# Kernel tuning notes

Measured on AMD Instinct MI355X. Metric: run time of the kernel, lower is better.

The kernel has to match this reference:

```python
import jax, jax.numpy as jnp
import numpy as np

B, L, D_MODEL, EXPAND, HEADDIM, QK_DIM = 2, 512, 512, 2, 128, 16
D_INNER = EXPAND * D_MODEL            # 1024
NHEADS = D_INNER // HEADDIM           # 8
EPS = 1e-3
STD_DEV = 1.0 / np.sqrt(2 * L * QK_DIM)
TWO_PI = 2.0 * np.pi


def setup_inputs() -> dict:
    key = jax.random.key(0)
    kv, kq, kk = jax.random.split(key, 3)
    v = jax.random.normal(kv, (B, L, D_INNER), dtype=jnp.float32)
    q = jax.random.normal(kq, (B, L, NHEADS * QK_DIM), dtype=jnp.float32)
    k = jax.random.normal(kk, (B, L, NHEADS * QK_DIM), dtype=jnp.float32)
    return {"v": v, "q": q, "k": k}


def reference(v, q, k):
    b, l, dim = v.shape
    residual = v
    # b l (n h) -> b l n h
    vh = v.reshape(b, l, NHEADS, HEADDIM)
    # b l (n d) -> b n d l
    qh = q.reshape(b, l, NHEADS, QK_DIM).transpose(0, 2, 3, 1)
    kh = k.reshape(b, l, NHEADS, QK_DIM).transpose(0, 2, 3, 1)
    pos = jnp.arange(l, dtype=v.dtype)  # position indices
    c = jnp.asarray(TWO_PI * EPS, dtype=v.dtype)
    # q_matrix[b,n,d,t,l] = cos(c * q[b,n,d,t] * pos[l])
    q_mat = jnp.cos(c * qh[:, :, :, :, None] * pos)
    # k_matrix[b,n,d,l,t] = cos(c * k[b,n,d,t] * pos[l])
    k_mat = jnp.cos(c * kh[:, :, :, None, :] * pos[:, None])
    sym = (q_mat - k_mat).sum(axis=2)  # (b, n, t, l)
    out = jnp.einsum('bntl,blnh->btnh', sym, vh)
    out = jnp.asarray(STD_DEV, v.dtype) * out
    return out.reshape(b, l, dim) + residual
```

## Files before the change

kernel.cpp:

```cpp
#include <hip/hip_runtime.h>

#define L_SEQ   512
#define NHEADS_ 8
#define HEADDIM_ 128
#define QKD     16
#define DINNER  1024
#define EPS_F   1e-3f
#define STD_F   0.0078125f

typedef __attribute__((ext_vector_type(8))) short  short8;
typedef __attribute__((ext_vector_type(4))) float  floatx4;

__device__ __forceinline__ float cosrev(float rev) {
    float r = rev - floorf(rev);
    return __builtin_amdgcn_cosf(r);
}

__device__ __forceinline__ unsigned short f2bf_rne(float x) {
    union { float f; unsigned int u; } v;
    v.f = x;
    unsigned int r = v.u + 0x7fffu + ((v.u >> 16) & 1u);
    return (unsigned short)(r >> 16);
}
__device__ __forceinline__ unsigned short f2bf_fast(float x) {
    union { float f; unsigned int u; } v;
    v.f = x;
    return (unsigned short)((v.u + 0x8000u) >> 16);
}

__global__ __launch_bounds__(256) void prep_kernel(const float* __restrict__ v,
                                                   const float* __restrict__ k,
                                                   unsigned short* __restrict__ vt,
                                                   float* __restrict__ ks) {
    const int bid = blockIdx.x;
    const int tid = threadIdx.x;
    if (bid < 512) {
        const int bn = bid & 15, tc = (bid >> 4) & 15, lh = bid >> 8;
        const int b = bn >> 3, n = bn & 7;
        const int l = lh * 256 + tid;
        const float t0f = (float)(tc * 32);
        const float* krow = k + ((size_t)(b * L_SEQ + l)) * (NHEADS_ * QKD) + n * QKD;
        float M[16], C1[16], C0[16];
#pragma unroll
        for (int d4 = 0; d4 < 4; ++d4) {
            float4 kk = *(const float4*)(krow + 4 * d4);
            float dl[4] = {EPS_F * kk.x, EPS_F * kk.y, EPS_F * kk.z, EPS_F * kk.w};
#pragma unroll
            for (int e = 0; e < 4; ++e) {
                int d = d4 * 4 + e;
                M[d]  = 2.f * cosrev(dl[e]);
                C1[d] = cosrev(dl[e] * t0f);
                C0[d] = cosrev(dl[e] * (t0f - 1.f));
            }
        }
        float* kout = ks + ((size_t)bn * L_SEQ) * L_SEQ + (size_t)(tc * 32) * L_SEQ + l;
#pragma unroll
        for (int m = 0; m < 32; ++m) {
            float s0 = (C1[0] + C1[1]) + (C1[2] + C1[3]);
            float s1 = (C1[4] + C1[5]) + (C1[6] + C1[7]);
            float s2 = (C1[8] + C1[9]) + (C1[10] + C1[11]);
            float s3 = (C1[12] + C1[13]) + (C1[14] + C1[15]);
            kout[(size_t)m * L_SEQ] = (s0 + s1) + (s2 + s3);
#pragma unroll
            for (int d = 0; d < 16; ++d) {
                float nx = fmaf(M[d], C1[d], -C0[d]);
                C0[d] = C1[d];
                C1[d] = nx;
            }
        }
    } else {
        const int bid2 = bid - 512;
        const int l0 = (bid2 & 7) * 64;
        const int h0 = ((bid2 >> 3) & 1) * 64;
        const int bn = bid2 >> 4;
        const int b = bn >> 3, n = bn & 7;
        __shared__ float tile[64][65];
        const float* vb = v + ((size_t)b * L_SEQ) * DINNER + n * HEADDIM_;
#pragma unroll
        for (int i = 0; i < 16; ++i) {
            int f = i * 256 + tid;
            int hh = f & 63, ll = f >> 6;
            tile[hh][ll] = vb[(size_t)(l0 + ll) * DINNER + (h0 + hh)];
        }
        __syncthreads();
        unsigned short* vrow = vt + ((size_t)bn * HEADDIM_) * L_SEQ;
#pragma unroll
        for (int i = 0; i < 16; ++i) {
            int f = i * 256 + tid;
            int ll = f & 63, hh = f >> 6;
            vrow[(size_t)(h0 + hh) * L_SEQ + (l0 + ll)] = f2bf_rne(tile[hh][ll]);
        }
    }
}

__global__ __launch_bounds__(256, 2) void vand_main(const float* __restrict__ v,
                                                    const float* __restrict__ q,
                                                    const unsigned short* __restrict__ vt,
                                                    const float* __restrict__ ks,
                                                    float* __restrict__ out) {
    const int tid  = threadIdx.x;
    const int w    = tid >> 6;
    const int lane = tid & 63;
    const int tl   = lane & 15;
    const int quad = lane >> 4;
    const int ttile = blockIdx.x;
    const int bn    = blockIdx.y;
    const int b = bn >> 3, n = bn & 7;

    const int   t   = ttile * 16 + tl;
    const int   l0  = w * 128 + quad * 32;
    const float l0f = (float)l0;

    const float* qrow = q + ((size_t)(b * L_SEQ + t)) * (NHEADS_ * QKD) + n * QKD;
    float M[16], C1[16], C0[16];
#pragma unroll
    for (int d4 = 0; d4 < 4; ++d4) {
        float4 qq = *(const float4*)(qrow + 4 * d4);
        float dl[4] = {EPS_F * qq.x, EPS_F * qq.y, EPS_F * qq.z, EPS_F * qq.w};
#pragma unroll
        for (int e = 0; e < 4; ++e) {
            int d = d4 * 4 + e;
            M[d]  = 2.f * cosrev(dl[e]);
            C1[d] = cosrev(dl[e] * l0f);
            C0[d] = cosrev(dl[e] * (l0f - 1.f));
        }
    }

    const unsigned short* vrow  = vt + ((size_t)bn * HEADDIM_) * L_SEQ;
    const float*          ksrow = ks + ((size_t)(bn * L_SEQ + t)) * L_SEQ + l0;

    floatx4 acc[8] = {};

#pragma unroll
    for (int c = 0; c < 4; ++c) {
        float4 kv0 = *(const float4*)(ksrow + c * 8);
        float4 kv1 = *(const float4*)(ksrow + c * 8 + 4);
        const float kvv[8] = {kv0.x, kv0.y, kv0.z, kv0.w, kv1.x, kv1.y, kv1.z, kv1.w};
        short8 af;
#pragma unroll
        for (int jj = 0; jj < 8; ++jj) {
            float s0 = (C1[0] + C1[1]) + (C1[2] + C1[3]);
            float s1 = (C1[4] + C1[5]) + (C1[6] + C1[7]);
            float s2 = (C1[8] + C1[9]) + (C1[10] + C1[11]);
            float s3 = (C1[12] + C1[13]) + (C1[14] + C1[15]);
            float s  = ((s0 + s1) + (s2 + s3)) - kvv[jj];
            af[jj] = (short)f2bf_fast(s);
#pragma unroll
            for (int d = 0; d < 16; ++d) {
                float nx = fmaf(M[d], C1[d], -C0[d]);
                C0[d] = C1[d];
                C1[d] = nx;
            }
        }
#pragma unroll
        for (int ht = 0; ht < 8; ++ht) {
            const short8 bfr = *(const short8*)((const short*)vrow +
                                  (size_t)(ht * 16 + tl) * L_SEQ + l0 + c * 8);
            acc[ht] = __builtin_amdgcn_mfma_f32_16x16x32_bf16(af, bfr, acc[ht], 0, 0, 0);
        }
    }

    __shared__ float red[4][64][33];
#pragma unroll
    for (int ht = 0; ht < 8; ++ht)
#pragma unroll
        for (int r = 0; r < 4; ++r)
            red[w][lane][ht * 4 + r] = acc[ht][r];
    __syncthreads();

    const float* vbase = v   + ((size_t)b * L_SEQ) * DINNER + n * HEADDIM_;
    float*       obase = out + ((size_t)b * L_SEQ) * DINNER + n * HEADDIM_;
#pragma unroll
    for (int i = 0; i < 8; ++i) {
        int e    = i * 256 + tid;
        int h    = e & 127;
        int tloc = e >> 7;
        int lidx = ((tloc >> 2) << 4) + (h & 15);
        int aidx = ((h >> 4) << 2) + (tloc & 3);
        float sum = red[0][lidx][aidx] + red[1][lidx][aidx]
                  + red[2][lidx][aidx] + red[3][lidx][aidx];
        size_t gi = (size_t)(ttile * 16 + tloc) * DINNER + h;
        obase[gi] = vbase[gi] + STD_F * sum;
    }
}

extern "C" void kernel_launch(void* const* d_in, const int* in_sizes, int n_in,
                              void* d_out, int out_size, void* d_ws, size_t ws_size,
                              hipStream_t stream) {
    const float* v = (const float*)d_in[0];
    const float* q = (const float*)d_in[1];
    const float* k = (const float*)d_in[2];
    float* out = (float*)d_out;
    unsigned short* vt = (unsigned short*)d_ws;
    float* ks = (float*)((char*)d_ws + (2u << 20));

    prep_kernel<<<dim3(768), 256, 0, stream>>>(v, k, vt, ks);
    vand_main<<<dim3(L_SEQ / 16, 16), 256, 0, stream>>>(v, q, vt, ks, out);
}
```

Before: 84.79 us.

## Fuse k-cosine sum into main kernel via LDS and use packed float2 recurrences

Removes the global ks intermediate, about 16 MB of fp32 written and then read back. Each main block now computes its own 16 rows of the k-side cosine sums into padded shared memory. The Chebyshev recurrences are rewritten on float2 vectors so the compiler can emit packed FMA instructions. In exchange, k-side work is recomputed per block tile and LDS use grows by about 34 KB, which may reduce occupancy.

Result: faster. 77.31 us (-8.8%).

```diff
diff --git a/kernel.cpp b/kernel.cpp
--- a/kernel.cpp
+++ b/kernel.cpp
@@ -8,8 +8,11 @@
 #define EPS_F   1e-3f
 #define STD_F   0.0078125f
 
+#define KS_ROW  529
+
 typedef __attribute__((ext_vector_type(8))) short  short8;
 typedef __attribute__((ext_vector_type(4))) float  floatx4;
+typedef __attribute__((ext_vector_type(2))) float  float2v;
 
 __device__ __forceinline__ float cosrev(float rev) {
     float r = rev - floorf(rev);
@@ -28,76 +31,37 @@
     return (unsigned short)((v.u + 0x8000u) >> 16);
 }
 
-__global__ __launch_bounds__(256) void prep_kernel(const float* __restrict__ v,
-                                                   const float* __restrict__ k,
-                                                   unsigned short* __restrict__ vt,
-                                                   float* __restrict__ ks) {
+__global__ __launch_bounds__(256) void vtrans_kernel(const float* __restrict__ v,
+                                                     unsigned short* __restrict__ vt) {
     const int bid = blockIdx.x;
     const int tid = threadIdx.x;
-    if (bid < 512) {
-        const int bn = bid & 15, tc = (bid >> 4) & 15, lh = bid >> 8;
-        const int b = bn >> 3, n = bn & 7;
-        const int l = lh * 256 + tid;
-        const float t0f = (float)(tc * 32);
-        const float* krow = k + ((size_t)(b * L_SEQ + l)) * (NHEADS_ * QKD) + n * QKD;
-        float M[16], C1[16], C0[16];
+    const int l0 = (bid & 7) * 64;
+    const int h0 = ((bid >> 3) & 1) * 64;
+    const int bn = bid >> 4;
+    const int b = bn >> 3, n = bn & 7;
+    __shared__ float tile[64][65];
+    const float* vb = v + ((size_t)b * L_SEQ) * DINNER + n * HEADDIM_;
 #pragma unroll
-        for (int d4 = 0; d4 < 4; ++d4) {
-            float4 kk = *(const float4*)(krow + 4 * d4);
-            float dl[4] = {EPS_F * kk.x, EPS_F * kk.y, EPS_F * kk.z, EPS_F * kk.w};
+    for (int i = 0; i < 16; ++i) {
+        int f = i * 256 + tid;
+        int hh = f & 63, ll = f >> 6;
+        tile[hh][ll] = vb[(size_t)(l0 + ll) * DINNER + (h0 + hh)];
+    }
+    __syncthreads();
+    unsigned short* vrow = vt + ((size_t)bn * HEADDIM_) * L_SEQ;
 #pragma unroll
-            for (int e = 0; e < 4; ++e) {
-                int d = d4 * 4 + e;
-                M[d]  = 2.f * cosrev(dl[e]);
-                C1[d] = cosrev(dl[e] * t0f);
-                C0[d] = cosrev(dl[e] * (t0f - 1.f));
-            }
-        }
-        float* kout = ks + ((size_t)bn * L_SEQ) * L_SEQ + (size_t)(tc * 32) * L_SEQ + l;
-#pragma unroll
-        for (int m = 0; m < 32; ++m) {
-            float s0 = (C1[0] + C1[1]) + (C1[2] + C1[3]);
-            float s1 = (C1[4] + C1[5]) + (C1[6] + C1[7]);
-            float s2 = (C1[8] + C1[9]) + (C1[10] + C1[11]);
-            float s3 = (C1[12] + C1[13]) + (C1[14] + C1[15]);
-            kout[(size_t)m * L_SEQ] = (s0 + s1) + (s2 + s3);
-#pragma unroll
-            for (int d = 0; d < 16; ++d) {
-                float nx = fmaf(M[d], C1[d], -C0[d]);
-                C0[d] = C1[d];
-                C1[d] = nx;
-            }
-        }
-    } else {
-        const int bid2 = bid - 512;
-        const int l0 = (bid2 & 7) * 64;
-        const int h0 = ((bid2 >> 3) & 1) * 64;
-        const int bn = bid2 >> 4;
-        const int b = bn >> 3, n = bn & 7;
-        __shared__ float tile[64][65];
-        const float* vb = v + ((size_t)b * L_SEQ) * DINNER + n * HEADDIM_;
-#pragma unroll
-        for (int i = 0; i < 16; ++i) {
-            int f = i * 256 + tid;
-            int hh = f & 63, ll = f >> 6;
-            tile[hh][ll] = vb[(size_t)(l0 + ll) * DINNER + (h0 + hh)];
-        }
-        __syncthreads();
-        unsigned short* vrow = vt + ((size_t)bn * HEADDIM_) * L_SEQ;
-#pragma unroll
-        for (int i = 0; i < 16; ++i) {
-            int f = i * 256 + tid;
-            int ll = f & 63, hh = f >> 6;
-            vrow[(size_t)(h0 + hh) * L_SEQ + (l0 + ll)] = f2bf_rne(tile[hh][ll]);
-        }
+    for (int i = 0; i < 16; ++i) {
+        int f = i * 256 + tid;
+        int ll = f & 63, hh = f >> 6;
+        vrow[(size_t)(h0 + hh) * L_SEQ + (l0 + ll)] = f2bf_rne(tile[hh][ll]);
     }
 }
 
-__global__ __launch_bounds__(256, 2) void vand_main(const float* __restrict__ v,
-                                                    const float* __restrict__ q,
-                                                    const unsigned short* __restrict__ vt,
-                                                    const float* __restrict__ ks,
-                                                    float* __restrict__ out) {
+__global__ __launch_bounds__(256, 2) void vand_fused(const float* __restrict__ v,
+                                                     const float* __restrict__ q,
+                                                     const float* __restrict__ k,
+                                                     const unsigned short* __restrict__ vt,
+                                                     float* __restrict__ out) {
     const int tid  = threadIdx.x;
     const int w    = tid >> 6;
     const int lane = tid & 63;
@@ -106,50 +70,88 @@
     const int ttile = blockIdx.x;
     const int bn    = blockIdx.y;
     const int b = bn >> 3, n = bn & 7;
+    const float t0f = (float)(ttile * 16);
+
+    __shared__ float ksl[16 * KS_ROW];
+    __shared__ float red[4][64][33];
+
+#pragma unroll
+    for (int rep = 0; rep < 2; ++rep) {
+        const int l = tid + rep * 256;
+        const float* krow = k + ((size_t)(b * L_SEQ + l)) * (NHEADS_ * QKD) + n * QKD;
+        float kk[16];
+#pragma unroll
+        for (int d4 = 0; d4 < 4; ++d4) {
+            float4 t4 = *(const float4*)(krow + 4 * d4);
+            kk[d4 * 4 + 0] = t4.x; kk[d4 * 4 + 1] = t4.y;
+            kk[d4 * 4 + 2] = t4.z; kk[d4 * 4 + 3] = t4.w;
+        }
+        float2v M2[8], C1[8], C0[8];
+#pragma unroll
+        for (int i = 0; i < 8; ++i) {
+            float a0 = EPS_F * kk[2 * i], a1 = EPS_F * kk[2 * i + 1];
+            M2[i].x = 2.f * cosrev(a0);          M2[i].y = 2.f * cosrev(a1);
+            C1[i].x = cosrev(a0 * t0f);          C1[i].y = cosrev(a1 * t0f);
+            C0[i].x = cosrev(a0 * (t0f - 1.f));  C0[i].y = cosrev(a1 * (t0f - 1.f));
+        }
+        const int base = (l >> 5) * 33 + (l & 31);
+#pragma unroll
+        for (int m = 0; m < 16; ++m) {
+            float2v s = ((C1[0] + C1[1]) + (C1[2] + C1[3]))
+                      + ((C1[4] + C1[5]) + (C1[6] + C1[7]));
+            ksl[m * KS_ROW + base] = s.x + s.y;
+#pragma unroll
+            for (int i = 0; i < 8; ++i) {
+                float2v nx = M2[i] * C1[i] - C0[i];
+                C0[i] = C1[i];
+                C1[i] = nx;
+            }
+        }
+    }
+    __syncthreads();
 
     const int   t   = ttile * 16 + tl;
     const int   l0  = w * 128 + quad * 32;
     const float l0f = (float)l0;
 
     const float* qrow = q + ((size_t)(b * L_SEQ + t)) * (NHEADS_ * QKD) + n * QKD;
-    float M[16], C1[16], C0[16];
+    float2v M2[8], C1[8], C0[8];
 #pragma unroll
     for (int d4 = 0; d4 < 4; ++d4) {
         float4 qq = *(const float4*)(qrow + 4 * d4);
-        float dl[4] = {EPS_F * qq.x, EPS_F * qq.y, EPS_F * qq.z, EPS_F * qq.w};
+        float aa[4] = {EPS_F * qq.x, EPS_F * qq.y, EPS_F * qq.z, EPS_F * qq.w};
 #pragma unroll
-        for (int e = 0; e < 4; ++e) {
-            int d = d4 * 4 + e;
-            M[d]  = 2.f * cosrev(dl[e]);
-            C1[d] = cosrev(dl[e] * l0f);
-            C0[d] = cosrev(dl[e] * (l0f - 1.f));
+        for (int e = 0; e < 2; ++e) {
+            int i = d4 * 2 + e;
+            float a0 = aa[2 * e], a1 = aa[2 * e + 1];
+            M2[i].x = 2.f * cosrev(a0);          M2[i].y = 2.f * cosrev(a1);
+            C1[i].x = cosrev(a0 * l0f);          C1[i].y = cosrev(a1 * l0f);
+            C0[i].x = cosrev(a0 * (l0f - 1.f));  C0[i].y = cosrev(a1 * (l0f - 1.f));
         }
     }
 
-    const unsigned short* vrow  = vt + ((size_t)bn * HEADDIM_) * L_SEQ;
-    const float*          ksrow = ks + ((size_t)(bn * L_SEQ + t)) * L_SEQ + l0;
+    const unsigned short* vrow = vt + ((size_t)bn * HEADDIM_) * L_SEQ;
+    const int klds = tl * KS_ROW + (4 * w + quad) * 33;
 
     floatx4 acc[8] = {};
 
 #pragma unroll
     for (int c = 0; c < 4; ++c) {
-        float4 kv0 = *(const float4*)(ksrow + c * 8);
-        float4 kv1 = *(const float4*)(ksrow + c * 8 + 4);
-        const float kvv[8] = {kv0.x, kv0.y, kv0.z, kv0.w, kv1.x, kv1.y, kv1.z, kv1.w};
+        float kv[8];
+#pragma unroll
+        for (int jj = 0; jj < 8; ++jj) kv[jj] = ksl[klds + c * 8 + jj];
         short8 af;
 #pragma unroll
         for (int jj = 0; jj < 8; ++jj) {
-            float s0 = (C1[0] + C1[1]) + (C1[2] + C1[3]);
-            float s1 = (C1[4] + C1[5]) + (C1[6] + C1[7]);
-            float s2 = (C1[8] + C1[9]) + (C1[10] + C1[11]);
-            float s3 = (C1[12] + C1[13]) + (C1[14] + C1[15]);
-            float s  = ((s0 + s1) + (s2 + s3)) - kvv[jj];
+            float2v sv = ((C1[0] + C1[1]) + (C1[2] + C1[3]))
+                       + ((C1[4] + C1[5]) + (C1[6] + C1[7]));
+            float s = (sv.x + sv.y) - kv[jj];
             af[jj] = (short)f2bf_fast(s);
 #pragma unroll
-            for (int d = 0; d < 16; ++d) {
-                float nx = fmaf(M[d], C1[d], -C0[d]);
-                C0[d] = C1[d];
-                C1[d] = nx;
+            for (int i = 0; i < 8; ++i) {
+                float2v nx = M2[i] * C1[i] - C0[i];
+                C0[i] = C1[i];
+                C1[i] = nx;
             }
         }
 #pragma unroll
@@ -160,7 +162,6 @@
         }
     }
 
-    __shared__ float red[4][64][33];
 #pragma unroll
     for (int ht = 0; ht < 8; ++ht)
 #pragma unroll
@@ -192,8 +193,7 @@
     const float* k = (const float*)d_in[2];
     float* out = (float*)d_out;
     unsigned short* vt = (unsigned short*)d_ws;
-    float* ks = (float*)((char*)d_ws + (2u << 20));
 
-    prep_kernel<<<dim3(768), 256, 0, stream>>>(v, k, vt, ks);
-    vand_main<<<dim3(L_SEQ / 16, 16), 256, 0, stream>>>(v, q, vt, ks, out);
+    vtrans_kernel<<<dim3(256), 256, 0, stream>>>(v, vt);
+    vand_fused<<<dim3(L_SEQ / 16, 16), 256, 0, stream>>>(v, q, k, vt, out);
 }
```
